# Kernel optimization log

Hardware: AMD Instinct MI355X
Metric: run time of the kernel (lower is better)

## Reference

```python
import jax, jax.numpy as jnp
import numpy as np

H, D = 16, 64  # heads, head dim; E = H*D


def setup_inputs() -> dict:
    key = jax.random.key(0)
    ks = jax.random.split(key, 8)
    B, T, E = 4, 1024, 1024
    s = (2.0 / E) ** 0.5
    return {
        "x": jax.random.normal(ks[0], (B, T, E), jnp.float32),
        "wq": jax.random.normal(ks[1], (H * D, E), jnp.float32) * s,
        "wk": jax.random.normal(ks[2], (H * D, E), jnp.float32) * s,
        "wv": jax.random.normal(ks[3], (H * D, E), jnp.float32) * s,
        "wvr": jax.random.normal(ks[4], (H * D, E), jnp.float32) * s,
        "wr": jax.random.normal(ks[5], (H, E, T), jnp.float32) * s,
        "wj": jax.random.normal(ks[6], (E, E), jnp.float32) * s,
        "gate": jnp.zeros((H, 3), jnp.float32),
        "wo": jax.random.normal(ks[7], (E, H * D), jnp.float32) * s,
    }


def reference(x, wq, wk, wv, wvr, wr, wj, gate, wo):
    B, T, E = x.shape
    scale = 1.0 / D ** 0.5

    def proj(w):  # torch Linear: y = x @ w.T, then split heads -> (B,H,T,D)
        return jnp.einsum('bte,fe->btf', x, w).reshape(B, T, H, D).transpose(0, 2, 1, 3)

    mask = jnp.triu(jnp.ones((T, T), bool), 1)  # True above diagonal (masked)

    # --- branch 1: standard causal QKV attention ---
    q, k, v = proj(wq), proj(wk), proj(wv)
    s1 = jnp.einsum('bhid,bhjd->bhij', q, k) * scale
    a1 = jax.nn.softmax(jnp.where(mask, -jnp.inf, s1), axis=-1)
    out1 = jnp.einsum('bhij,bhjd->bhid', a1, v)

    # --- branch 2: RRPRAM (parameter-based per-key scores, broadcast over queries) ---
    rv = proj(wvr)
    s2 = jnp.einsum('bte,het->bht', x, wr[:, :, :T]) * scale  # score per key position
    s2 = jnp.broadcast_to(s2[:, :, None, :], (B, H, T, T))
    a2 = jax.nn.softmax(jnp.where(mask, -jnp.inf, s2), axis=-1)
    out2 = jnp.einsum('bhij,bhjd->bhid', a2, rv)

    # --- branch 3: Janus self-echo (rank-1 outer-product scores) ---
    echo = jnp.einsum('bte,fe->btf', x, wj)            # x @ wj.T
    echo_back = jnp.einsum('btf,fe->bte', echo, wj)    # echo @ wj
    sc = jnp.sum(x * echo_back, axis=-1) / (E ** 0.5)  # (B,T)
    s3 = sc[:, :, None] * sc[:, None, :]               # (B,T,T)
    a3 = jax.nn.softmax(jnp.where(mask, -jnp.inf, s3), axis=-1)
    jv = echo.reshape(B, T, H, D).transpose(0, 2, 1, 3)
    out3 = jnp.einsum('bij,bhjd->bhid', a3, jv)

    # --- gated combine (softmax over the 3 branches per head) ---
    g = jax.nn.softmax(gate, axis=-1)  # (H,3)
    out = (g[:, 0][None, :, None, None] * out1
           + g[:, 1][None, :, None, None] * out2
           + g[:, 2][None, :, None, None] * out3)
    out = out.transpose(0, 2, 1, 3).reshape(B, T, H * D)
    return jnp.einsum('btf,ef->bte', out, wo)
```

## Files before the change

kernel.cpp:

```cpp
#include <hip/hip_runtime.h>
#include <cstdint>
#include <cstddef>

typedef unsigned short u16;
typedef short bf16x8 __attribute__((ext_vector_type(8)));
typedef short bf16x4 __attribute__((ext_vector_type(4)));
typedef float f32x4 __attribute__((ext_vector_type(4)));

constexpr int B_ = 4, T_ = 1024, E_ = 1024, H_ = 16, D_ = 64;

__device__ __forceinline__ float bf2f(u16 u) {
  union { unsigned u; float f; } v; v.u = ((unsigned)u) << 16; return v.f;
}
__device__ __forceinline__ u16 f2bf(float f) {
  union { float f; unsigned u; } v; v.f = f;
  return (u16)((v.u + 0x7fffu + ((v.u >> 16) & 1u)) >> 16);
}

#define GLD_LDS16(gp, lp)                                                      \
  __builtin_amdgcn_global_load_lds(                                            \
      (const __attribute__((address_space(1))) void*)(gp),                     \
      (__attribute__((address_space(3))) void*)(lp), 16, 0, 0)

#define SBAR()                                                                 \
  do {                                                                         \
    __builtin_amdgcn_sched_barrier(0);                                         \
    __builtin_amdgcn_s_barrier();                                              \
    __builtin_amdgcn_sched_barrier(0);                                         \
  } while (0)
#define WAIT_LGKM0()                                                           \
  do {                                                                         \
    asm volatile("s_waitcnt lgkmcnt(0)" ::: "memory");                         \
    __builtin_amdgcn_sched_barrier(0);                                         \
  } while (0)
#define WAIT_VM4()                                                             \
  do {                                                                         \
    asm volatile("s_waitcnt vmcnt(4)" ::: "memory");                           \
    __builtin_amdgcn_sched_barrier(0);                                         \
  } while (0)

__global__ __launch_bounds__(512, 2) void gemm_qkv8(
    const u16* __restrict__ A, const u16* __restrict__ Bm, u16* __restrict__ C)
{
  __shared__ u16 smem[65536];

  const int tid  = threadIdx.x;
  const int lane = tid & 63;
  const int wave = tid >> 6;
  const int wm = wave >> 2;
  const int wn = wave & 3;
  const int fr = lane & 15;
  const int fg = lane >> 4;
  const int fx = fr & 7;
  const int m0 = blockIdx.y * 256;
  const int n0 = blockIdx.x * 256;

  auto stage = [&](int ktl, int half) {
    const int buf = ktl & 1;
    int kt = (ktl > 15) ? 15 : ktl;
    const int k0 = kt << 6;
    const u16* src = (half < 2)
        ? (A  + (size_t)(m0 + (half & 1) * 128) * 1024)
        : (Bm + (size_t)(n0 + (half & 1) * 128) * 1024);
    u16* dst = smem + (buf << 15) + (half << 13);
    #pragma unroll
    for (int l = 0; l < 2; l++) {
      const int s = (l << 9) | tid;
      const int r = s >> 3, ch = s & 7;
      GLD_LDS16(src + (size_t)r * 1024 + k0 + ((ch ^ (r & 7)) << 3), dst + s * 8);
    }
  };

  f32x4 acc[8][4];
  #pragma unroll
  for (int i = 0; i < 8; i++)
    #pragma unroll
    for (int j = 0; j < 4; j++) acc[i][j] = f32x4{0.f, 0.f, 0.f, 0.f};

  stage(0, 0); stage(0, 1); stage(0, 2); stage(0, 3);
  stage(1, 2); stage(1, 0);
  WAIT_VM4();
  __builtin_amdgcn_s_barrier();
  __builtin_amdgcn_sched_barrier(0);

  const int ko0 = (fg ^ fx) << 3;
  const int ko1 = ((4 | fg) ^ fx) << 3;

  for (int t = 0; t < 16; t++) {
    const int buf = t & 1;
    const int ab = (buf << 15) + (wm << 13) + fr * 64;
    const int bb = (buf << 15) + 16384 + (wn << 12) + fr * 64;

    bf16x8 aF[4][2], bF[4][2];

    #pragma unroll
    for (int mt = 0; mt < 4; mt++) {
      aF[mt][0] = *(const bf16x8*)(smem + ab + mt * 1024 + ko0);
      aF[mt][1] = *(const bf16x8*)(smem + ab + mt * 1024 + ko1);
    }
    #pragma unroll
    for (int nt = 0; nt < 2; nt++) {
      bF[nt][0] = *(const bf16x8*)(smem + bb + nt * 1024 + ko0);
      bF[nt][1] = *(const bf16x8*)(smem + bb + nt * 1024 + ko1);
    }
    stage(t + 1, 1);
    SBAR();
    WAIT_LGKM0();
    __builtin_amdgcn_s_setprio(1);
    #pragma unroll
    for (int mt = 0; mt < 4; mt++)
      #pragma unroll
      for (int nt = 0; nt < 2; nt++) {
        acc[mt][nt] = __builtin_amdgcn_mfma_f32_16x16x32_bf16(aF[mt][0], bF[nt][0], acc[mt][nt], 0, 0, 0);
        acc[mt][nt] = __builtin_amdgcn_mfma_f32_16x16x32_bf16(aF[mt][1], bF[nt][1], acc[mt][nt], 0, 0, 0);
      }
    __builtin_amdgcn_s_setprio(0);
    SBAR();

    #pragma unroll
    for (int nt = 2; nt < 4; nt++) {
      bF[nt][0] = *(const bf16x8*)(smem + bb + nt * 1024 + ko0);
      bF[nt][1] = *(const bf16x8*)(smem + bb + nt * 1024 + ko1);
    }
    stage(t + 1, 3);
    SBAR();
    WAIT_LGKM0();
    __builtin_amdgcn_s_setprio(1);
    #pragma unroll
    for (int mt = 0; mt < 4; mt++)
      #pragma unroll
      for (int nt = 2; nt < 4; nt++) {
        acc[mt][nt] = __builtin_amdgcn_mfma_f32_16x16x32_bf16(aF[mt][0], bF[nt][0], acc[mt][nt], 0, 0, 0);
        acc[mt][nt] = __builtin_amdgcn_mfma_f32_16x16x32_bf16(aF[mt][1], bF[nt][1], acc[mt][nt], 0, 0, 0);
      }
    __builtin_amdgcn_s_setprio(0);
    SBAR();

    #pragma unroll
    for (int mt = 0; mt < 4; mt++) {
      aF[mt][0] = *(const bf16x8*)(smem + ab + (4 + mt) * 1024 + ko0);
      aF[mt][1] = *(const bf16x8*)(smem + ab + (4 + mt) * 1024 + ko1);
    }
    stage(t + 2, 2);
    SBAR();
    WAIT_LGKM0();
    __builtin_amdgcn_s_setprio(1);
    #pragma unroll
    for (int mt = 0; mt < 4; mt++)
      #pragma unroll
      for (int nt = 0; nt < 2; nt++) {
        acc[4 + mt][nt] = __builtin_amdgcn_mfma_f32_16x16x32_bf16(aF[mt][0], bF[nt][0], acc[4 + mt][nt], 0, 0, 0);
        acc[4 + mt][nt] = __builtin_amdgcn_mfma_f32_16x16x32_bf16(aF[mt][1], bF[nt][1], acc[4 + mt][nt], 0, 0, 0);
      }
    __builtin_amdgcn_s_setprio(0);
    SBAR();

    stage(t + 2, 0);
    SBAR();
    __builtin_amdgcn_s_setprio(1);
    #pragma unroll
    for (int mt = 0; mt < 4; mt++)
      #pragma unroll
      for (int nt = 2; nt < 4; nt++) {
        acc[4 + mt][nt] = __builtin_amdgcn_mfma_f32_16x16x32_bf16(aF[mt][0], bF[nt][0], acc[4 + mt][nt], 0, 0, 0);
        acc[4 + mt][nt] = __builtin_amdgcn_mfma_f32_16x16x32_bf16(aF[mt][1], bF[nt][1], acc[4 + mt][nt], 0, 0, 0);
      }
    __builtin_amdgcn_s_setprio(0);
    WAIT_VM4();
    __builtin_amdgcn_s_barrier();
    __builtin_amdgcn_sched_barrier(0);
  }

  u16* Cp = C + (size_t)(m0 + wm * 128) * 4096 + n0 + wn * 64;
  #pragma unroll
  for (int mt = 0; mt < 8; mt++)
    #pragma unroll
    for (int nt = 0; nt < 4; nt++)
      #pragma unroll
      for (int r2 = 0; r2 < 4; r2++)
        Cp[(size_t)(mt * 16 + fg * 4 + r2) * 4096 + nt * 16 + fr] = f2bf(acc[mt][nt][r2]);
}

template<int WM, int WN, int MT, int NT, bool CBF16>
__global__ __launch_bounds__(WM * WN * 64) void gemm_bt(
    const u16* __restrict__ A, const u16* __restrict__ Bm,
    void* __restrict__ Cv, int N, int K,
    int lda, int ldb, int ldc,
    long batchA, long batchB, long batchC, float alpha)
{
  constexpr int TM = WM * MT * 16;
  constexpr int TN = WN * NT * 16;
  constexpr int THREADS = WM * WN * 64;
  constexpr int ASZ = TM * 32, BSZ = TN * 32;

  __shared__ u16 smem[ASZ + BSZ];
  u16* sA = smem;
  u16* sB = smem + ASZ;

  const int z = blockIdx.z;
  const u16* Ab = A + (size_t)z * batchA;
  const u16* Bb = Bm + (size_t)z * batchB;
  const int m0 = blockIdx.y * TM;
  const int n0 = blockIdx.x * TN;
  const int tid = threadIdx.x;
  const int lane = tid & 63;
  const int wave = tid >> 6;
  const int wm = wave % WM;
  const int wn = wave / WM;
  const int fr = lane & 15;
  const int fg = lane >> 4;

  f32x4 acc[MT][NT];
  const f32x4 zero = {0.f, 0.f, 0.f, 0.f};
  #pragma unroll
  for (int i = 0; i < MT; i++)
    #pragma unroll
    for (int j = 0; j < NT; j++) acc[i][j] = zero;

  for (int k0 = 0; k0 < K; k0 += 32) {
    __syncthreads();
    for (int s = tid; s < TM * 4; s += THREADS) {
      const int row = s >> 2, ch = s & 3;
      GLD_LDS16(Ab + (size_t)(m0 + row) * lda + k0 + ch * 8, &sA[s * 8]);
    }
    for (int s = tid; s < TN * 4; s += THREADS) {
      const int row = s >> 2, ch = s & 3;
      int rr = n0 + row; if (rr > N - 1) rr = N - 1;
      GLD_LDS16(Bb + (size_t)rr * ldb + k0 + ch * 8, &sB[s * 8]);
    }
    __syncthreads();

    bf16x8 av[MT], bv[NT];
    #pragma unroll
    for (int mt = 0; mt < MT; mt++)
      av[mt] = *(const bf16x8*)&sA[((wm * MT + mt) * 16 + fr) * 32 + fg * 8];
    #pragma unroll
    for (int nt = 0; nt < NT; nt++)
      bv[nt] = *(const bf16x8*)&sB[((wn * NT + nt) * 16 + fr) * 32 + fg * 8];
    #pragma unroll
    for (int mt = 0; mt < MT; mt++)
      #pragma unroll
      for (int nt = 0; nt < NT; nt++)
        acc[mt][nt] = __builtin_amdgcn_mfma_f32_16x16x32_bf16(av[mt], bv[nt], acc[mt][nt], 0, 0, 0);
  }

  const int er = (lane >> 4) * 4;
  const int ec = lane & 15;
  #pragma unroll
  for (int mt = 0; mt < MT; mt++) {
    #pragma unroll
    for (int nt = 0; nt < NT; nt++) {
      const int row = m0 + (wm * MT + mt) * 16 + er;
      const int col = n0 + (wn * NT + nt) * 16 + ec;
      if (col < N) {
        #pragma unroll
        for (int r2 = 0; r2 < 4; r2++) {
          const float vv = acc[mt][nt][r2] * alpha;
          const size_t ci = (size_t)z * batchC + (size_t)(row + r2) * ldc + col;
          if constexpr (CBF16) ((u16*)Cv)[ci] = f2bf(vv);
          else                 ((float*)Cv)[ci] = vv;
        }
      }
    }
  }
}

__global__ __launch_bounds__(256) void gemm_echo(
    const u16* __restrict__ A, const u16* __restrict__ Alo,
    const u16* __restrict__ Bm, const u16* __restrict__ Blo,
    u16* __restrict__ echoT, float* __restrict__ sc)
{
  constexpr int TM = 128, TN = 64;
  constexpr int ASZ = TM * 32, BSZ = TN * 32;
  __shared__ u16 smem[2 * (ASZ + BSZ)];
  u16* sA  = smem;
  u16* sB  = smem + ASZ;
  u16* sAl = smem + ASZ + BSZ;
  u16* sBl = smem + 2 * ASZ + BSZ;

  const int m0 = blockIdx.y * TM;
  const int n0 = blockIdx.x * TN;
  const int tid = threadIdx.x;
  const int lane = tid & 63;
  const int wave = tid >> 6;
  const int wm = wave % 2;
  const int wn = wave / 2;
  const int fr = lane & 15, fg = lane >> 4;

  f32x4 acc[4][2];
  #pragma unroll
  for (int i = 0; i < 4; i++)
    #pragma unroll
    for (int j = 0; j < 2; j++) acc[i][j] = f32x4{0.f, 0.f, 0.f, 0.f};

  for (int k0 = 0; k0 < E_; k0 += 32) {
    __syncthreads();
    for (int s = tid; s < TM * 4; s += 256) {
      const int row = s >> 2, ch = s & 3;
      const size_t go = (size_t)(m0 + row) * E_ + k0 + ch * 8;
      GLD_LDS16(A + go, &sA[s * 8]);
      GLD_LDS16(Alo + go, &sAl[s * 8]);
    }
    for (int s = tid; s < TN * 4; s += 256) {
      const int row = s >> 2, ch = s & 3;
      const size_t go = (size_t)(n0 + row) * E_ + k0 + ch * 8;
      GLD_LDS16(Bm + go, &sB[s * 8]);
      GLD_LDS16(Blo + go, &sBl[s * 8]);
    }
    __syncthreads();

    bf16x8 av[4], bv[2], al[4], bl[2];
    #pragma unroll
    for (int mt = 0; mt < 4; mt++) {
      av[mt] = *(const bf16x8*)&sA[((wm * 4 + mt) * 16 + fr) * 32 + fg * 8];
      al[mt] = *(const bf16x8*)&sAl[((wm * 4 + mt) * 16 + fr) * 32 + fg * 8];
    }
    #pragma unroll
    for (int nt = 0; nt < 2; nt++) {
      bv[nt] = *(const bf16x8*)&sB[((wn * 2 + nt) * 16 + fr) * 32 + fg * 8];
      bl[nt] = *(const bf16x8*)&sBl[((wn * 2 + nt) * 16 + fr) * 32 + fg * 8];
    }
    #pragma unroll
    for (int mt = 0; mt < 4; mt++)
      #pragma unroll
      for (int nt = 0; nt < 2; nt++) {
        acc[mt][nt] = __builtin_amdgcn_mfma_f32_16x16x32_bf16(av[mt], bv[nt], acc[mt][nt], 0, 0, 0);
        acc[mt][nt] = __builtin_amdgcn_mfma_f32_16x16x32_bf16(al[mt], bv[nt], acc[mt][nt], 0, 0, 0);
        acc[mt][nt] = __builtin_amdgcn_mfma_f32_16x16x32_bf16(av[mt], bl[nt], acc[mt][nt], 0, 0, 0);
      }
  }

  __syncthreads();
  const int b   = m0 >> 10;
  const int t0l = m0 & 1023;
  const int ec  = lane & 15;
  u16* lt = smem;

  #pragma unroll
  for (int mt = 0; mt < 4; mt++) {
    float sq[4] = {0.f, 0.f, 0.f, 0.f};
    #pragma unroll
    for (int nt = 0; nt < 2; nt++) {
      const int cl = (wn * 2 + nt) * 16 + ec;
      #pragma unroll
      for (int r2 = 0; r2 < 4; r2++) {
        const float vv = acc[mt][nt][r2];
        sq[r2] += vv * vv;
        lt[cl * 132 + (wm * 4 + mt) * 16 + fg * 4 + r2] = f2bf(vv);
      }
    }
    #pragma unroll
    for (int m2 = 1; m2 < 16; m2 <<= 1) {
      sq[0] += __shfl_xor(sq[0], m2, 64);
      sq[1] += __shfl_xor(sq[1], m2, 64);
      sq[2] += __shfl_xor(sq[2], m2, 64);
      sq[3] += __shfl_xor(sq[3], m2, 64);
    }
    if (ec == 0) {
      #pragma unroll
      for (int r2 = 0; r2 < 4; r2++)
        atomicAdd(&sc[(size_t)b * T_ + t0l + (wm * 4 + mt) * 16 + fg * 4 + r2], sq[r2]);
    }
  }
  __syncthreads();
  for (int s = tid; s < 64 * 128; s += 256) {
    const int f = s >> 7, t = s & 127;
    echoT[((size_t)b * E_ + n0 + f) * T_ + t0l + t] = lt[f * 132 + t];
  }
}

__global__ __launch_bounds__(256, 2) void flash1(
    const u16* __restrict__ qkvr, const u16* __restrict__ vTb, u16* __restrict__ out1) {
  const int it = blockIdx.x, h = blockIdx.y, b = blockIdx.z;
  const int tid = threadIdx.x, lane = tid & 63, w = tid >> 6;
  const int fr = lane & 15, fg = lane >> 4;

  __shared__ u16 sQ[8192];
  __shared__ u16 sK[8192];
  __shared__ u16 sV[8192];

  const u16* Qb = qkvr + ((size_t)(b * T_) + it * 128) * 4096 + h * 64;
  const u16* Kb = qkvr + (size_t)(b * T_) * 4096 + 1024 + h * 64;
  const u16* Vb = vTb + (size_t)(b * H_ + h) * (D_ * T_);

  for (int s = tid; s < 1024; s += 256) {
    const int l = s & 63, g = s >> 6;
    const int row = (g >> 1) * 16 + (l & 15);
    const int c8  = (g & 1) * 4 + (l >> 4);
    GLD_LDS16(Qb + (size_t)row * 4096 + c8 * 8, &sQ[s * 8]);
  }
  __syncthreads();

  bf16x8 bQ[2][2];
  #pragma unroll
  for (int mf = 0; mf < 2; mf++)
    #pragma unroll
    for (int kk = 0; kk < 2; kk++)
      bQ[mf][kk] = *(const bf16x8*)&sQ[((((w * 2 + mf) * 2 + kk) << 6) | lane) * 8];

  f32x4 accO[2][4];
  float mrow[2], lrow[2];
  #pragma unroll
  for (int mf = 0; mf < 2; mf++) {
    mrow[mf] = -3.0e38f; lrow[mf] = 0.f;
    #pragma unroll
    for (int nd = 0; nd < 4; nd++) accO[mf][nd] = f32x4{0.f, 0.f, 0.f, 0.f};
  }

  for (int jt = 0; jt <= it; jt++) {
    __syncthreads();
    for (int s = tid; s < 1024; s += 256) {
      const int l = s & 63, g = s >> 6;
      const int row = (g >> 1) * 16 + (l & 15);
      const int c8  = (g & 1) * 4 + (l >> 4);
      GLD_LDS16(Kb + (size_t)(jt * 128 + row) * 4096 + c8 * 8, &sK[s * 8]);
    }
    for (int s = tid; s < 1024; s += 256) {
      const int jc = s >> 6, d = s & 63;
      GLD_LDS16(Vb + ((size_t)(jt * 16 + jc)) * 512 + d * 8, &sV[s * 8]);
    }
    __syncthreads();

    f32x4 accST[2][8];
    #pragma unroll
    for (int mf = 0; mf < 2; mf++)
      #pragma unroll
      for (int nf = 0; nf < 8; nf++) accST[mf][nf] = f32x4{0.f, 0.f, 0.f, 0.f};
    #pragma unroll
    for (int kk = 0; kk < 2; kk++) {
      #pragma unroll
      for (int nf = 0; nf < 8; nf++) {
        const bf16x8 aK = *(const bf16x8*)&sK[((((nf << 1) | kk) << 6) | lane) * 8];
        accST[0][nf] = __builtin_amdgcn_mfma_f32_16x16x32_bf16(aK, bQ[0][kk], accST[0][nf], 0, 0, 0);
        accST[1][nf] = __builtin_amdgcn_mfma_f32_16x16x32_bf16(aK, bQ[1][kk], accST[1][nf], 0, 0, 0);
      }
    }

    const bool diag = (jt == it);
    bf16x4 pf[2][8];
    #pragma unroll
    for (int mf = 0; mf < 2; mf++) {
      const int iloc = w * 32 + mf * 16 + fr;
      float sv[8][4];
      float rmax = -3.0e38f;
      #pragma unroll
      for (int nf = 0; nf < 8; nf++)
        #pragma unroll
        for (int r = 0; r < 4; r++) {
          float s = accST[mf][nf][r] * 0.125f;
          if (diag && (nf * 16 + fg * 4 + r) > iloc) s = -3.0e38f;
          sv[nf][r] = s;
          rmax = fmaxf(rmax, s);
        }
      rmax = fmaxf(rmax, __shfl_xor(rmax, 16, 64));
      rmax = fmaxf(rmax, __shfl_xor(rmax, 32, 64));
      const float mn = fmaxf(mrow[mf], rmax);
      const float al = __expf(mrow[mf] - mn);
      mrow[mf] = mn;
      float ps = 0.f;
      #pragma unroll
      for (int nf = 0; nf < 8; nf++)
        #pragma unroll
        for (int r = 0; r < 4; r++) {
          const float pv = __expf(sv[nf][r] - mn);
          ps += pv;
          pf[mf][nf][r] = (short)f2bf(pv);
        }
      ps += __shfl_xor(ps, 16, 64);
      ps += __shfl_xor(ps, 32, 64);
      lrow[mf] = lrow[mf] * al + ps;
      #pragma unroll
      for (int r = 0; r < 4; r++) {
        const float alr = __shfl(al, fg * 4 + r, 64);
        #pragma unroll
        for (int nd = 0; nd < 4; nd++) accO[mf][nd][r] *= alr;
      }
    }

    #pragma unroll
    for (int kc = 0; kc < 8; kc++) {
      bf16x8 bV[4];
      #pragma unroll
      for (int nd = 0; nd < 4; nd++) {
        const bf16x4 vv = *(const bf16x4*)&sV[
            (((kc * 2 + (fg >> 1)) * 64 + nd * 16 + fr) * 8) + (fg & 1) * 4];
        bV[nd] = bf16x8{vv[0], vv[1], vv[2], vv[3], 0, 0, 0, 0};
      }
      #pragma unroll
      for (int mf = 0; mf < 2; mf++) {
        const bf16x4 pp = pf[mf][kc];
        const bf16x8 pA = bf16x8{pp[0], pp[1], pp[2], pp[3], 0, 0, 0, 0};
        #pragma unroll
        for (int nd = 0; nd < 4; nd++)
          accO[mf][nd] = __builtin_amdgcn_mfma_f32_16x16x32_bf16(pA, bV[nd], accO[mf][nd], 0, 0, 0);
      }
    }
  }

  u16* op = out1 + ((size_t)(b * T_) + it * 128) * E_ + h * 64;
  #pragma unroll
  for (int mf = 0; mf < 2; mf++) {
    const float li = 1.0f / lrow[mf];
    #pragma unroll
    for (int r = 0; r < 4; r++) {
      const float linv = __shfl(li, fg * 4 + r, 64);
      const int row = w * 32 + mf * 16 + fg * 4 + r;
      #pragma unroll
      for (int nd = 0; nd < 4; nd++)
        op[(size_t)row * E_ + nd * 16 + fr] = f2bf(accO[mf][nd][r] * linv);
    }
  }
}

__device__ __forceinline__ float block_max256(float v, float* red) {
  #pragma unroll
  for (int m = 32; m > 0; m >>= 1) v = fmaxf(v, __shfl_xor(v, m, 64));
  if ((threadIdx.x & 63) == 0) red[threadIdx.x >> 6] = v;
  __syncthreads();
  const float r = fmaxf(fmaxf(red[0], red[1]), fmaxf(red[2], red[3]));
  __syncthreads();
  return r;
}
__device__ __forceinline__ float block_sum256(float v, float* red) {
  #pragma unroll
  for (int m = 32; m > 0; m >>= 1) v += __shfl_xor(v, m, 64);
  if ((threadIdx.x & 63) == 0) red[threadIdx.x >> 6] = v;
  __syncthreads();
  const float r = (red[0] + red[1]) + (red[2] + red[3]);
  __syncthreads();
  return r;
}

__global__ __launch_bounds__(256) void cast_all(
    const float* __restrict__ x, const float* __restrict__ wq,
    const float* __restrict__ wk, const float* __restrict__ wv,
    const float* __restrict__ wvr, const float* __restrict__ wo,
    const float* __restrict__ wj,
    u16* __restrict__ xb, u16* __restrict__ xlo, u16* __restrict__ wcat,
    u16* __restrict__ wob, u16* __restrict__ wjb, u16* __restrict__ wjlo) {
  const int bid = blockIdx.x;
  if (bid < 4096) {
    const size_t i = ((size_t)bid * 256 + threadIdx.x) * 4;
    const float4 v = *(const float4*)(x + i);
    ushort4 oh, ol;
    oh.x = f2bf(v.x); ol.x = f2bf(v.x - bf2f(oh.x));
    oh.y = f2bf(v.y); ol.y = f2bf(v.y - bf2f(oh.y));
    oh.z = f2bf(v.z); ol.z = f2bf(v.z - bf2f(oh.z));
    oh.w = f2bf(v.w); ol.w = f2bf(v.w - bf2f(oh.w));
    *(ushort4*)(xb + i) = oh;
    *(ushort4*)(xlo + i) = ol;
  } else if (bid < 8192) {
    const int r = (bid - 4096) >> 10;
    const float* src = (r == 0) ? wq : (r == 1) ? wk : (r == 2) ? wv : wvr;
    const size_t i = ((size_t)((bid - 4096) & 1023) * 256 + threadIdx.x) * 4;
    const float4 v = *(const float4*)(src + i);
    ushort4 o;
    o.x = f2bf(v.x); o.y = f2bf(v.y); o.z = f2bf(v.z); o.w = f2bf(v.w);
    *(ushort4*)(wcat + (size_t)r * (1 << 20) + i) = o;
  } else if (bid < 9216) {
    const size_t i = ((size_t)(bid - 8192) * 256 + threadIdx.x) * 4;
    const float4 v = *(const float4*)(wo + i);
    ushort4 o;
    o.x = f2bf(v.x); o.y = f2bf(v.y); o.z = f2bf(v.z); o.w = f2bf(v.w);
    *(ushort4*)(wob + i) = o;
  } else {
    const size_t i = ((size_t)(bid - 9216) * 256 + threadIdx.x) * 4;
    const float4 v = *(const float4*)(wj + i);
    ushort4 oh, ol;
    oh.x = f2bf(v.x); ol.x = f2bf(v.x - bf2f(oh.x));
    oh.y = f2bf(v.y); ol.y = f2bf(v.y - bf2f(oh.y));
    oh.z = f2bf(v.z); ol.z = f2bf(v.z - bf2f(oh.z));
    oh.w = f2bf(v.w); ol.w = f2bf(v.w - bf2f(oh.w));
    *(ushort4*)(wjb + i) = oh;
    *(ushort4*)(wjlo + i) = ol;
  }
}

__global__ __launch_bounds__(256) void s2_direct(
    const u16* __restrict__ xb, const float* __restrict__ wr, float* __restrict__ s2) {
  const int t0 = blockIdx.x * 32, h = blockIdx.y;
  const int tt = threadIdx.x & 31, eg = threadIdx.x >> 5;
  float acc[4] = {0.f, 0.f, 0.f, 0.f};
  const float* wp = wr + (size_t)h * E_ * T_ + t0 + tt;
  for (int ec = 0; ec < 8; ec++) {
    const int e0 = ec * 128 + eg * 16;
    bf16x8 xv[4][2];
    #pragma unroll
    for (int b = 0; b < 4; b++) {
      const u16* xp = xb + ((size_t)(b * T_) + t0 + tt) * E_ + e0;
      xv[b][0] = *(const bf16x8*)xp;
      xv[b][1] = *(const bf16x8*)(xp + 8);
    }
    #pragma unroll
    for (int e2 = 0; e2 < 16; e2++) {
      const float w = wp[(size_t)(e0 + e2) * T_];
      #pragma unroll
      for (int b = 0; b < 4; b++)
        acc[b] += bf2f((u16)xv[b][e2 >> 3][e2 & 7]) * w;
    }
  }
  __shared__ float red[8][4][33];
  #pragma unroll
  for (int b = 0; b < 4; b++) red[eg][b][tt] = acc[b];
  __syncthreads();
  if (threadIdx.x < 128) {
    const int b = threadIdx.x >> 5, t = threadIdx.x & 31;
    float s = 0.f;
    #pragma unroll
    for (int g = 0; g < 8; g++) s += red[g][b][t];
    s2[((size_t)b * H_ + h) * T_ + t0 + t] = s * 0.125f;
  }
}

__global__ __launch_bounds__(256) void a3_softmax(const float* __restrict__ sc, u16* __restrict__ a3) {
  const int i = blockIdx.x;
  const int b = blockIdx.y;
  const float* sr = sc + (size_t)b * T_;
  const float sci = sr[i] * 0.03125f;
  u16* row = a3 + ((size_t)b * T_ + i) * T_;
  __shared__ float red[4];
  float v[4];
  float m = -3.0e38f;
  #pragma unroll
  for (int k = 0; k < 4; k++) {
    const int j = threadIdx.x + k * 256;
    const float xv = (j <= i) ? sci * (sr[j] * 0.03125f) : -3.0e38f;
    v[k] = xv;
    m = fmaxf(m, xv);
  }
  m = block_max256(m, red);
  float s = 0.f;
  #pragma unroll
  for (int k = 0; k < 4; k++) {
    const int j = threadIdx.x + k * 256;
    const float p = (j <= i) ? __expf(v[k] - m) : 0.f;
    v[k] = p;
    s += p;
  }
  s = block_sum256(s, red);
  const float inv = 1.0f / s;
  #pragma unroll
  for (int k = 0; k < 4; k++) {
    const int j = threadIdx.x + k * 256;
    row[j] = f2bf(v[k] * inv);
  }
}

__global__ __launch_bounds__(1024) void branch2_scan(
    const float* __restrict__ s2, const u16* __restrict__ rv, int ldrv,
    u16* __restrict__ out2) {
  const int h = blockIdx.x, b = blockIdx.y;
  const int tid = threadIdx.x;
  const int lane = tid & 63;
  const int wv = tid >> 6;

  const float* srow = s2 + ((size_t)b * H_ + h) * T_;

  __shared__ float wbuf[T_];
  __shared__ float numtot[16][64];
  __shared__ float dentot[16];
  __shared__ float redm[16];

  float m = srow[tid];
  #pragma unroll
  for (int mk = 32; mk > 0; mk >>= 1) m = fmaxf(m, __shfl_xor(m, mk, 64));
  if (lane == 0) redm[wv] = m;
  __syncthreads();
  m = redm[0];
  #pragma unroll
  for (int i2 = 1; i2 < 16; i2++) m = fmaxf(m, redm[i2]);

  wbuf[tid] = __expf(srow[tid] - m);
  __syncthreads();

  const u16* rvp = rv + (size_t)(b * T_) * ldrv + h * D_ + lane;
  const int j0 = wv * 64;
  float num = 0.f, den = 0.f;
  #pragma unroll 8
  for (int j2 = 0; j2 < 64; j2++) {
    const float w = wbuf[j0 + j2];
    den += w;
    num += w * bf2f(rvp[(size_t)(j0 + j2) * ldrv]);
  }
  numtot[wv][lane] = num;
  if (lane == 0) dentot[wv] = den;
  __syncthreads();

  float num_off = 0.f, den_off = 0.f;
  for (int w2 = 0; w2 < wv; w2++) {
    num_off += numtot[w2][lane];
    den_off += dentot[w2];
  }

  u16* op = out2 + (size_t)b * T_ * E_ + h * D_ + lane;
  num = num_off; den = den_off;
  #pragma unroll 8
  for (int j2 = 0; j2 < 64; j2++) {
    const float w = wbuf[j0 + j2];
    num += w * bf2f(rvp[(size_t)(j0 + j2) * ldrv]);
    den += w;
    op[(size_t)(j0 + j2) * E_] = f2bf(num / den);
  }
}

__global__ __launch_bounds__(256) void transpose_v(const u16* __restrict__ v, u16* __restrict__ vTb,
                                                   int ldv) {
  const int bh = blockIdx.x;
  const int b = bh >> 4, h = bh & 15;
  const int d0 = blockIdx.y * 32, t0 = blockIdx.z * 32;
  __shared__ u16 tile[32][33];
  const int c = threadIdx.x & 31, r0 = threadIdx.x >> 5;
  #pragma unroll
  for (int rr = 0; rr < 32; rr += 8) {
    const int t = t0 + rr + r0;
    tile[rr + r0][c] = v[((size_t)b * T_ + t) * ldv + h * 64 + d0 + c];
  }
  __syncthreads();
  #pragma unroll
  for (int rr = 0; rr < 32; rr += 8) {
    const int d = d0 + rr + r0;
    const int t = t0 + c;
    vTb[((size_t)(bh * 128 + (t >> 3)) * 64 + d) * 8 + (t & 7)] = tile[c][rr + r0];
  }
}

__global__ __launch_bounds__(256) void combine_gate(
    const u16* __restrict__ o1, const u16* __restrict__ o2, const u16* __restrict__ o3,
    const float* __restrict__ gate, u16* __restrict__ comb) {
  const size_t idx = (size_t)blockIdx.x * 256 + threadIdx.x;
  const int f = (int)(idx & (E_ - 1));
  const int h = f >> 6;
  const float g0 = gate[h * 3 + 0], g1 = gate[h * 3 + 1], g2 = gate[h * 3 + 2];
  const float mx = fmaxf(g0, fmaxf(g1, g2));
  const float e0 = __expf(g0 - mx), e1 = __expf(g1 - mx), e2 = __expf(g2 - mx);
  const float inv = 1.0f / (e0 + e1 + e2);
  const float o = (e0 * bf2f(o1[idx]) + e1 * bf2f(o2[idx]) + e2 * bf2f(o3[idx])) * inv;
  comb[idx] = f2bf(o);
}

extern "C" void kernel_launch(void* const* d_in, const int* in_sizes, int n_in,
                              void* d_out, int out_size, void* d_ws, size_t ws_size,
                              hipStream_t stream) {
  (void)in_sizes; (void)n_in; (void)out_size; (void)ws_size;
  const float* x    = (const float*)d_in[0];
  const float* wq   = (const float*)d_in[1];
  const float* wk   = (const float*)d_in[2];
  const float* wv   = (const float*)d_in[3];
  const float* wvr  = (const float*)d_in[4];
  const float* wr   = (const float*)d_in[5];
  const float* wj   = (const float*)d_in[6];
  const float* gate = (const float*)d_in[7];
  const float* wo   = (const float*)d_in[8];
  float* out = (float*)d_out;

  char* p = (char*)d_ws;
  auto alloc = [&](size_t bytes) -> char* {
    char* r = p; p += (bytes + 255) & ~(size_t)255; return r;
  };
  const size_t NTE = (size_t)B_ * T_ * E_;
  const size_t NW  = (size_t)E_ * E_;

  u16* xb    = (u16*)alloc(NTE * 2);
  u16* xlo   = (u16*)alloc(NTE * 2);
  u16* wcat  = (u16*)alloc(4 * NW * 2);
  u16* wjb   = (u16*)alloc(NW * 2);
  u16* wjlo  = (u16*)alloc(NW * 2);
  u16* wob   = (u16*)alloc(NW * 2);
  u16* qkvr  = (u16*)alloc(NTE * 4 * 2);
  u16* vT    = (u16*)alloc(NTE * 2);
  u16* echoT = (u16*)alloc(NTE * 2);
  u16* a3p   = (u16*)alloc(NTE * 2);
  float* sc  = (float*)alloc((size_t)B_ * T_ * 4);
  float* s2  = (float*)alloc((size_t)B_ * H_ * T_ * 4);
  u16* out1b = (u16*)alloc(NTE * 2);
  u16* out2b = (u16*)alloc(NTE * 2);
  u16* out3b = (u16*)alloc(NTE * 2);
  u16* comb  = (u16*)alloc(NTE * 2);

  cast_all<<<dim3(10240), 256, 0, stream>>>(x, wq, wk, wv, wvr, wo, wj,
                                            xb, xlo, wcat, wob, wjb, wjlo);
  hipMemsetAsync(sc, 0, (size_t)B_ * T_ * 4, stream);

  gemm_qkv8<<<dim3(16, 16), 512, 0, stream>>>(xb, wcat, qkvr);

  gemm_echo<<<dim3(16, 32, 1), 256, 0, stream>>>(xb, xlo, wjb, wjlo, echoT, sc);

  transpose_v<<<dim3(B_ * H_, D_ / 32, T_ / 32), 256, 0, stream>>>(qkvr + 2048, vT, 4096);
  s2_direct<<<dim3(T_ / 32, H_), 256, 0, stream>>>(xb, wr, s2);

  branch2_scan<<<dim3(H_, B_), 1024, 0, stream>>>(s2, qkvr + 3072, 4096, out2b);

  a3_softmax<<<dim3(T_, B_), 256, 0, stream>>>(sc, a3p);
  gemm_bt<2,2,4,2,true><<<dim3(E_ / 64, T_ / 128, B_), 256, 0, stream>>>(
      a3p, echoT, out3b, E_, T_, T_, T_, E_,
      (long)T_ * T_, (long)E_ * T_, (long)T_ * E_, 1.f);

  flash1<<<dim3(T_ / 128, H_, B_), 256, 0, stream>>>(qkvr, vT, out1b);

  combine_gate<<<dim3((unsigned)(NTE / 256)), 256, 0, stream>>>(out1b, out2b, out3b, gate, comb);
  gemm_bt<2,2,4,2,false><<<dim3(E_ / 64, (B_ * T_) / 128, 1), 256, 0, stream>>>(
      comb, wob, out, E_, E_, E_, E_, E_, 0L, 0L, 0L, 1.f);
}
```

Measured before the change: 375.9 us.

## Pair causal query tiles per block and double-buffer K/V loads in flash1

The causal attention kernel now processes two query tiles per block, tiles x and 7-x, so every block does the same number of key tiles. Blocks grow to 512 threads, with each of 8 waves owning 16 query rows. K/V tiles are double-buffered in LDS, and the next tile, or the second phase's Q and first K/V tile, is prefetched while the current one is computed. This targets causal load imbalance and exposed global-load latency, at the cost of more LDS per block and only 256 blocks in the grid.

```diff
diff --git a/kernel.cpp b/kernel.cpp
--- a/kernel.cpp
+++ b/kernel.cpp
@@ -369,145 +369,158 @@
   }
 }
 
-__global__ __launch_bounds__(256, 2) void flash1(
+__global__ __launch_bounds__(512, 2) void flash1p(
     const u16* __restrict__ qkvr, const u16* __restrict__ vTb, u16* __restrict__ out1) {
-  const int it = blockIdx.x, h = blockIdx.y, b = blockIdx.z;
+  const int x = blockIdx.x, h = blockIdx.y, b = blockIdx.z;
   const int tid = threadIdx.x, lane = tid & 63, w = tid >> 6;
   const int fr = lane & 15, fg = lane >> 4;
+  const int itA = x, itB = 7 - x;
 
   __shared__ u16 sQ[8192];
-  __shared__ u16 sK[8192];
-  __shared__ u16 sV[8192];
-
-  const u16* Qb = qkvr + ((size_t)(b * T_) + it * 128) * 4096 + h * 64;
+  __shared__ u16 sK[2][8192];
+  __shared__ u16 sV[2][8192];
+
   const u16* Kb = qkvr + (size_t)(b * T_) * 4096 + 1024 + h * 64;
   const u16* Vb = vTb + (size_t)(b * H_ + h) * (D_ * T_);
 
-  for (int s = tid; s < 1024; s += 256) {
-    const int l = s & 63, g = s >> 6;
-    const int row = (g >> 1) * 16 + (l & 15);
-    const int c8  = (g & 1) * 4 + (l >> 4);
-    GLD_LDS16(Qb + (size_t)row * 4096 + c8 * 8, &sQ[s * 8]);
-  }
-  __syncthreads();
-
-  bf16x8 bQ[2][2];
-  #pragma unroll
-  for (int mf = 0; mf < 2; mf++)
-    #pragma unroll
-    for (int kk = 0; kk < 2; kk++)
-      bQ[mf][kk] = *(const bf16x8*)&sQ[((((w * 2 + mf) * 2 + kk) << 6) | lane) * 8];
-
-  f32x4 accO[2][4];
-  float mrow[2], lrow[2];
-  #pragma unroll
-  for (int mf = 0; mf < 2; mf++) {
-    mrow[mf] = -3.0e38f; lrow[mf] = 0.f;
-    #pragma unroll
-    for (int nd = 0; nd < 4; nd++) accO[mf][nd] = f32x4{0.f, 0.f, 0.f, 0.f};
-  }
-
-  for (int jt = 0; jt <= it; jt++) {
-    __syncthreads();
-    for (int s = tid; s < 1024; s += 256) {
+  auto stageQ = [&](int it) {
+    const u16* Qb = qkvr + ((size_t)(b * T_) + it * 128) * 4096 + h * 64;
+    #pragma unroll
+    for (int s0 = 0; s0 < 1024; s0 += 512) {
+      const int s = s0 + tid;
       const int l = s & 63, g = s >> 6;
       const int row = (g >> 1) * 16 + (l & 15);
       const int c8  = (g & 1) * 4 + (l >> 4);
-      GLD_LDS16(Kb + (size_t)(jt * 128 + row) * 4096 + c8 * 8, &sK[s * 8]);
-    }
-    for (int s = tid; s < 1024; s += 256) {
+      GLD_LDS16(Qb + (size_t)row * 4096 + c8 * 8, &sQ[s * 8]);
+    }
+  };
+  auto stageKV = [&](int jt, int bi) {
+    #pragma unroll
+    for (int s0 = 0; s0 < 1024; s0 += 512) {
+      const int s = s0 + tid;
+      const int l = s & 63, g = s >> 6;
+      const int row = (g >> 1) * 16 + (l & 15);
+      const int c8  = (g & 1) * 4 + (l >> 4);
+      GLD_LDS16(Kb + (size_t)(jt * 128 + row) * 4096 + c8 * 8, &sK[bi][s * 8]);
+    }
+    #pragma unroll
+    for (int s0 = 0; s0 < 1024; s0 += 512) {
+      const int s = s0 + tid;
       const int jc = s >> 6, d = s & 63;
-      GLD_LDS16(Vb + ((size_t)(jt * 16 + jc)) * 512 + d * 8, &sV[s * 8]);
-    }
-    __syncthreads();
-
-    f32x4 accST[2][8];
-    #pragma unroll
-    for (int mf = 0; mf < 2; mf++)
-      #pragma unroll
-      for (int nf = 0; nf < 8; nf++) accST[mf][nf] = f32x4{0.f, 0.f, 0.f, 0.f};
-    #pragma unroll
-    for (int kk = 0; kk < 2; kk++) {
-      #pragma unroll
-      for (int nf = 0; nf < 8; nf++) {
-        const bf16x8 aK = *(const bf16x8*)&sK[((((nf << 1) | kk) << 6) | lane) * 8];
-        accST[0][nf] = __builtin_amdgcn_mfma_f32_16x16x32_bf16(aK, bQ[0][kk], accST[0][nf], 0, 0, 0);
-        accST[1][nf] = __builtin_amdgcn_mfma_f32_16x16x32_bf16(aK, bQ[1][kk], accST[1][nf], 0, 0, 0);
-      }
-    }
-
-    const bool diag = (jt == it);
-    bf16x4 pf[2][8];
-    #pragma unroll
-    for (int mf = 0; mf < 2; mf++) {
-      const int iloc = w * 32 + mf * 16 + fr;
+      GLD_LDS16(Vb + ((size_t)(jt * 16 + jc)) * 512 + d * 8, &sV[bi][s * 8]);
+    }
+  };
+
+  stageQ(itA);
+  stageKV(0, 0);
+  asm volatile("s_waitcnt vmcnt(0)" ::: "memory");
+  __syncthreads();
+
+  bf16x8 bQ[2];
+  f32x4 accO[4];
+  float mrow, lrow;
+
+  #pragma unroll 1
+  for (int ph = 0; ph < 2; ph++) {
+    const int it    = ph ? itB : itA;
+    const int sbase = ph ? (itA + 1) : 0;
+
+    #pragma unroll
+    for (int kk = 0; kk < 2; kk++)
+      bQ[kk] = *(const bf16x8*)&sQ[((((w * 2) + kk) << 6) | lane) * 8];
+    mrow = -3.0e38f; lrow = 0.f;
+    #pragma unroll
+    for (int nd = 0; nd < 4; nd++) accO[nd] = f32x4{0.f, 0.f, 0.f, 0.f};
+
+    for (int jt = 0; jt <= it; jt++) {
+      const int bi = (sbase + jt) & 1;
+
+      if (jt < it) {
+        stageKV(jt + 1, bi ^ 1);
+      } else if (ph == 0) {
+        stageQ(itB);
+        stageKV(0, bi ^ 1);
+      }
+
+      f32x4 accST[8];
+      #pragma unroll
+      for (int nf = 0; nf < 8; nf++) accST[nf] = f32x4{0.f, 0.f, 0.f, 0.f};
+      #pragma unroll
+      for (int kk = 0; kk < 2; kk++) {
+        #pragma unroll
+        for (int nf = 0; nf < 8; nf++) {
+          const bf16x8 aK = *(const bf16x8*)&sK[bi][((((nf << 1) | kk) << 6) | lane) * 8];
+          accST[nf] = __builtin_amdgcn_mfma_f32_16x16x32_bf16(aK, bQ[kk], accST[nf], 0, 0, 0);
+        }
+      }
+
+      const bool diag = (jt == it);
+      const int iloc = w * 16 + fr;
       float sv[8][4];
       float rmax = -3.0e38f;
       #pragma unroll
       for (int nf = 0; nf < 8; nf++)
         #pragma unroll
         for (int r = 0; r < 4; r++) {
-          float s = accST[mf][nf][r] * 0.125f;
+          float s = accST[nf][r] * 0.125f;
           if (diag && (nf * 16 + fg * 4 + r) > iloc) s = -3.0e38f;
           sv[nf][r] = s;
           rmax = fmaxf(rmax, s);
         }
       rmax = fmaxf(rmax, __shfl_xor(rmax, 16, 64));
       rmax = fmaxf(rmax, __shfl_xor(rmax, 32, 64));
-      const float mn = fmaxf(mrow[mf], rmax);
-      const float al = __expf(mrow[mf] - mn);
-      mrow[mf] = mn;
+      const float mn = fmaxf(mrow, rmax);
+      const float al = __expf(mrow - mn);
+      mrow = mn;
       float ps = 0.f;
+      bf16x4 pf[8];
       #pragma unroll
       for (int nf = 0; nf < 8; nf++)
         #pragma unroll
         for (int r = 0; r < 4; r++) {
           const float pv = __expf(sv[nf][r] - mn);
           ps += pv;
-          pf[mf][nf][r] = (short)f2bf(pv);
+          pf[nf][r] = (short)f2bf(pv);
         }
       ps += __shfl_xor(ps, 16, 64);
       ps += __shfl_xor(ps, 32, 64);
-      lrow[mf] = lrow[mf] * al + ps;
+      lrow = lrow * al + ps;
       #pragma unroll
       for (int r = 0; r < 4; r++) {
         const float alr = __shfl(al, fg * 4 + r, 64);
         #pragma unroll
-        for (int nd = 0; nd < 4; nd++) accO[mf][nd][r] *= alr;
-      }
-    }
-
-    #pragma unroll
-    for (int kc = 0; kc < 8; kc++) {
-      bf16x8 bV[4];
-      #pragma unroll
-      for (int nd = 0; nd < 4; nd++) {
-        const bf16x4 vv = *(const bf16x4*)&sV[
-            (((kc * 2 + (fg >> 1)) * 64 + nd * 16 + fr) * 8) + (fg & 1) * 4];
-        bV[nd] = bf16x8{vv[0], vv[1], vv[2], vv[3], 0, 0, 0, 0};
-      }
-      #pragma unroll
-      for (int mf = 0; mf < 2; mf++) {
-        const bf16x4 pp = pf[mf][kc];
+        for (int nd = 0; nd < 4; nd++) accO[nd][r] *= alr;
+      }
+
+      #pragma unroll
+      for (int kc = 0; kc < 8; kc++) {
+        bf16x8 bV[4];
+        #pragma unroll
+        for (int nd = 0; nd < 4; nd++) {
+          const bf16x4 vv = *(const bf16x4*)&sV[bi][
+              (((kc * 2 + (fg >> 1)) * 64 + nd * 16 + fr) * 8) + (fg & 1) * 4];
+          bV[nd] = bf16x8{vv[0], vv[1], vv[2], vv[3], 0, 0, 0, 0};
+        }
+        const bf16x4 pp = pf[kc];
         const bf16x8 pA = bf16x8{pp[0], pp[1], pp[2], pp[3], 0, 0, 0, 0};
         #pragma unroll
         for (int nd = 0; nd < 4; nd++)
-          accO[mf][nd] = __builtin_amdgcn_mfma_f32_16x16x32_bf16(pA, bV[nd], accO[mf][nd], 0, 0, 0);
-      }
-    }
-  }
-
-  u16* op = out1 + ((size_t)(b * T_) + it * 128) * E_ + h * 64;
-  #pragma unroll
-  for (int mf = 0; mf < 2; mf++) {
-    const float li = 1.0f / lrow[mf];
+          accO[nd] = __builtin_amdgcn_mfma_f32_16x16x32_bf16(pA, bV[nd], accO[nd], 0, 0, 0);
+      }
+
+      asm volatile("s_waitcnt vmcnt(0)" ::: "memory");
+      __syncthreads();
+    }
+
+    u16* op = out1 + ((size_t)(b * T_) + it * 128) * E_ + h * 64;
+    const float li = 1.0f / lrow;
     #pragma unroll
     for (int r = 0; r < 4; r++) {
       const float linv = __shfl(li, fg * 4 + r, 64);
-      const int row = w * 32 + mf * 16 + fg * 4 + r;
+      const int row = w * 16 + fg * 4 + r;
       #pragma unroll
       for (int nd = 0; nd < 4; nd++)
-        op[(size_t)row * E_ + nd * 16 + fr] = f2bf(accO[mf][nd][r] * linv);
+        op[(size_t)row * E_ + nd * 16 + fr] = f2bf(accO[nd][r] * linv);
     }
   }
 }
@@ -795,7 +808,7 @@
       a3p, echoT, out3b, E_, T_, T_, T_, E_,
       (long)T_ * T_, (long)E_ * T_, (long)T_ * E_, 1.f);
 
-  flash1<<<dim3(T_ / 128, H_, B_), 256, 0, stream>>>(qkvr, vT, out1b);
+  flash1p<<<dim3(4, H_, B_), 512, 0, stream>>>(qkvr, vT, out1b);
 
   combine_gate<<<dim3((unsigned)(NTE / 256)), 256, 0, stream>>>(out1b, out2b, out3b, gate, comb);
   gemm_bt<2,2,4,2,false><<<dim3(E_ / 64, (B_ * T_) / 128, 1), 256, 0, stream>>>(
```

After: 361.5 us. -3.8%, faster.
